# Kernel tuning notes

Hardware: AMD Instinct MI355X
Metric: run time of the kernel (lower is better)

Reference implementation:

```python
import jax, jax.numpy as jnp
import numpy as np
from jax import lax

D_INNER = 1024
D_STATE = 16
DT_RANK = 32


def conv2d(x, w, b, pad=1):
    y = lax.conv_general_dilated(x, w, (1, 1), [(pad, pad), (pad, pad)],
                                 dimension_numbers=('NCHW', 'OIHW', 'NCHW'))
    return y + b[None, :, None, None]


def maxpool2(x):
    return lax.reduce_window(x, -jnp.inf, lax.max, (1, 1, 2, 2), (1, 1, 2, 2), 'VALID')


def layer_norm(x, w, b, eps=1e-5):
    m = x.mean(-1, keepdims=True)
    v = ((x - m) ** 2).mean(-1, keepdims=True)
    return (x - m) * lax.rsqrt(v + eps) * w + b


def cblock(h, w1, b1, w2, b2):
    return jax.nn.relu(conv2d(jax.nn.relu(conv2d(h, w1, b1)), w2, b2))


def up2(d, w, b):
    # ConvTranspose2d(kernel=2, stride=2): each input pixel -> 2x2 output block
    Bn, Ci, H, W = d.shape
    y = jnp.einsum('bcij,copq->boipjq', d, w).reshape(Bn, w.shape[1], 2 * H, 2 * W)
    return y + b[None, :, None, None]


def eblock(e, d, upw, upb, w1, b1, w2, b2):
    d = up2(d, upw, upb)
    dy = e.shape[2] - d.shape[2]
    dx = e.shape[3] - d.shape[3]
    e = e[:, :, dy // 2:e.shape[2] - dy // 2, dx // 2:e.shape[3] - dx // 2]
    return cblock(jnp.concatenate([e, d], 1), w1, b1, w2, b2)


def mamba(hs, inW, cw, cb, xpW, dtW, dtB, Alog, Dp, outW):
    # standard Mamba-1 mixer: in_proj -> causal depthwise conv -> selective scan -> gate -> out_proj
    Bn, L, _ = hs.shape
    xz = jnp.einsum('bld,ed->ble', hs, inW)                       # [B,L,2*d_inner]
    xi, z = xz[..., :D_INNER], xz[..., D_INNER:]
    xc = lax.conv_general_dilated(xi.transpose(0, 2, 1), cw[:, None, :], (1,), [(3, 0)],
                                  dimension_numbers=('NCH', 'OIH', 'NCH'),
                                  feature_group_count=D_INNER)    # causal, len L
    xc = jax.nn.silu(xc + cb[None, :, None]).transpose(0, 2, 1)   # [B,L,d_inner]
    xdbl = jnp.einsum('bld,ed->ble', xc, xpW)                     # [B,L,dt_rank+2*d_state]
    dt = jax.nn.softplus(jnp.einsum('blr,dr->bld', xdbl[..., :DT_RANK], dtW) + dtB)
    Bs = xdbl[..., DT_RANK:DT_RANK + D_STATE]
    Cs = xdbl[..., DT_RANK + D_STATE:]
    A = -jnp.exp(Alog)                                            # [d_inner,d_state]
    dA = jnp.exp(dt[..., None] * A)                               # [B,L,d_inner,d_state]
    dBu = (dt * xc)[..., None] * Bs[:, :, None, :]

    def step(h, inp):
        dA_t, dBu_t, C_t = inp
        h = dA_t * h + dBu_t
        return h, jnp.einsum('bdn,bn->bd', h, C_t)

    h0 = jnp.zeros((Bn, D_INNER, D_STATE), hs.dtype)
    _, ys = lax.scan(step, h0, (dA.transpose(1, 0, 2, 3), dBu.transpose(1, 0, 2, 3), Cs.transpose(1, 0, 2)))
    y = ys.transpose(1, 0, 2) + Dp * xc
    return jnp.einsum('ble,de->bld', y * jax.nn.silu(z), outW)


def setup_inputs() -> dict:
    key = jax.random.key(0)
    ks = iter(jax.random.split(key, 80))

    def w(shape, fan_in):
        return jax.random.normal(next(ks), shape, jnp.float32) * np.float32(np.sqrt(2.0 / fan_in))

    H = W = 128
    fy = np.fft.fftfreq(H)
    fx = np.fft.fftfreq(W)
    r = np.sqrt(fy[:, None] ** 2 + fx[None, :] ** 2)
    r = r / r.max()
    bands = [(0.0, 0.15), (0.15, 0.35), (0.35, 1.0001)]
    freq_masks = jnp.asarray(np.stack([((r >= lo) & (r < hi)).astype(np.float32) for lo, hi in bands]))

    d = {}
    d['x'] = jax.random.normal(next(ks), (2, 1, H, W), jnp.float32)
    d['freq_masks'] = freq_masks
    for ci, co, n in [(3, 64, 'e1'), (64, 128, 'e2'), (128, 256, 'e3'), (256, 512, 'e4')]:
        d[n + 'w1'] = w((co, ci, 3, 3), ci * 9)
        d[n + 'b1'] = jnp.zeros((co,), jnp.float32)
        d[n + 'w2'] = w((co, co, 3, 3), co * 9)
        d[n + 'b2'] = jnp.zeros((co,), jnp.float32)
    d['cls_token'] = jnp.zeros((1, 1, 512), jnp.float32)
    d['norm_w'] = jnp.ones((24, 512), jnp.float32)
    d['norm_b'] = jnp.zeros((24, 512), jnp.float32)
    d['in_proj_w'] = w((24, 2048, 512), 512)
    d['conv1d_w'] = w((24, 1024, 4), 4)
    d['conv1d_b'] = jnp.zeros((24, 1024), jnp.float32)
    d['x_proj_w'] = w((24, 64, 1024), 1024)
    d['dt_w'] = w((24, 1024, 32), 32)
    d['dt_b'] = jnp.full((24, 1024), float(np.log(np.expm1(0.01))), jnp.float32)
    d['A_log'] = jnp.broadcast_to(jnp.log(jnp.arange(1, 17, dtype=jnp.float32)), (24, 1024, 16)) + 0.0
    d['D_ssm'] = jnp.ones((24, 1024), jnp.float32)
    d['out_proj_w'] = w((24, 512, 1024), 1024)
    for n, ci, co, cc in [('d4', 512, 256, 768), ('d3', 256, 128, 384), ('d2', 128, 64, 192), ('d1', 64, 32, 96)]:
        d[n + 'up_w'] = w((ci, co, 2, 2), ci * 4)
        d[n + 'up_b'] = jnp.zeros((co,), jnp.float32)
        d[n + 'w1'] = w((co, cc, 3, 3), cc * 9)
        d[n + 'b1'] = jnp.zeros((co,), jnp.float32)
        d[n + 'w2'] = w((co, co, 3, 3), co * 9)
        d[n + 'b2'] = jnp.zeros((co,), jnp.float32)
    d['final_w'] = w((4, 32, 1, 1), 32)
    d['final_b'] = jnp.zeros((4,), jnp.float32)
    return d


def reference(x, freq_masks, e1w1, e1b1, e1w2, e1b2, e2w1, e2b1, e2w2, e2b2,
              e3w1, e3b1, e3w2, e3b2, e4w1, e4b1, e4w2, e4b2, cls_token,
              norm_w, norm_b, in_proj_w, conv1d_w, conv1d_b, x_proj_w, dt_w, dt_b,
              A_log, D_ssm, out_proj_w,
              d4up_w, d4up_b, d4w1, d4b1, d4w2, d4b2,
              d3up_w, d3up_b, d3w1, d3b1, d3w2, d3b2,
              d2up_w, d2up_b, d2w1, d2b1, d2w2, d2b2,
              d1up_w, d1up_b, d1w1, d1b1, d1w2, d1b2,
              final_w, final_b):
    # DCT/FFT frequency split: [B,1,H,W] -> [B,3,H,W]
    xf = jnp.fft.fft2(x)
    x_freq = jnp.real(jnp.fft.ifft2(xf * freq_masks[None]))

    e1 = cblock(x_freq, e1w1, e1b1, e1w2, e1b2); p1 = maxpool2(e1)
    e2 = cblock(p1, e2w1, e2b1, e2w2, e2b2); p2 = maxpool2(e2)
    e3 = cblock(p2, e3w1, e3b1, e3w2, e3b2); p3 = maxpool2(e3)
    e4 = cblock(p3, e4w1, e4b1, e4w2, e4b2); p4 = maxpool2(e4)   # [B,512,H/16,W/16]

    Bn, _, Hs, Ws = p4.shape
    seq = p4.reshape(Bn, 512, Hs * Ws).transpose(0, 2, 1)
    tok = jnp.concatenate([jnp.broadcast_to(cls_token, (Bn, 1, 512)), seq], 1)

    params = (norm_w, norm_b, in_proj_w, conv1d_w, conv1d_b, x_proj_w, dt_w, dt_b, A_log, D_ssm, out_proj_w)

    def layer(carry, p):
        hidden, residual = carry
        nw, nb, inW, cw, cb, xpW, dtW, dtB, Alog, Dp, outW = p
        residual = residual + hidden   # first block: residual starts == hidden (faithful)
        hs = layer_norm(residual, nw, nb)
        hs = mamba(hs, inW, cw, cb, xpW, dtW, dtB, Alog, Dp, outW)
        return (hs, residual), None

    (hidden, _), _ = lax.scan(layer, (tok, tok), params)

    xsp = hidden[:, 1:, :].transpose(0, 2, 1).reshape(Bn, 512, Hs, Ws)

    d4 = eblock(e4, xsp, d4up_w, d4up_b, d4w1, d4b1, d4w2, d4b2)
    d3 = eblock(e3, d4, d3up_w, d3up_b, d3w1, d3b1, d3w2, d3b2)
    d2 = eblock(e2, d3, d2up_w, d2up_b, d2w1, d2b1, d2w2, d2b2)
    d1 = eblock(e1, d2, d1up_w, d1up_b, d1w1, d1b1, d1w2, d1b2)

    out = conv2d(d1, final_w, final_b, pad=0)
    out = jax.image.resize(out, (out.shape[0], out.shape[1], out.shape[2] * 16, out.shape[3] * 16), 'bilinear')
    return out
```

## Files before the change

kernel.cpp:

```cpp
#include <hip/hip_runtime.h>
#include <math.h>

#define PI_F 3.14159265358979323846f
typedef _Float16 f16;
typedef __attribute__((ext_vector_type(8))) _Float16 f16x8;
typedef __attribute__((ext_vector_type(4))) float f32x4;

__device__ __forceinline__ float siluf(float x){ return x / (1.f + expf(-x)); }
__device__ __forceinline__ float softplusf(float x){ return fmaxf(x,0.f) + log1pf(expf(-fabsf(x))); }
__device__ __forceinline__ void f2hl(float v, f16& hi, f16& lo){
  hi = (f16)v;
  lo = (f16)(v - (float)hi);
}

__global__ void k_dft_rows(const float* __restrict__ x, float* __restrict__ Tre, float* __restrict__ Tim){
  int v = threadIdx.x; int y = blockIdx.x; int b = blockIdx.y;
  __shared__ float cs[128], sn[128];
  float ang = -2.f*PI_F*(float)v/128.f;
  cs[v]=cosf(ang); sn[v]=sinf(ang);
  __syncthreads();
  const float* row = x + (b*128+y)*128;
  float re=0.f, im=0.f;
  for(int n=0;n<128;n++){ float xv=row[n]; int ph=(v*n)&127; re=fmaf(xv,cs[ph],re); im=fmaf(xv,sn[ph],im); }
  int o=(b*128+y)*128+v; Tre[o]=re; Tim[o]=im;
}
__global__ void k_dft_cols(const float* __restrict__ Tre, const float* __restrict__ Tim,
                           float* __restrict__ Fre, float* __restrict__ Fim){
  int v=threadIdx.x; int u=blockIdx.x; int b=blockIdx.y;
  __shared__ float cs[128], sn[128];
  float ang=-2.f*PI_F*(float)v/128.f; cs[v]=cosf(ang); sn[v]=sinf(ang);
  __syncthreads();
  float re=0.f,im=0.f;
  for(int y=0;y<128;y++){
    int ph=(u*y)&127; float c=cs[ph], s=sn[ph];
    int o=(b*128+y)*128+v;
    float tr=Tre[o], ti=Tim[o];
    re += tr*c - ti*s; im += tr*s + ti*c;
  }
  int o=(b*128+u)*128+v; Fre[o]=re; Fim[o]=im;
}
__global__ void k_idft_cols(const float* __restrict__ Fre,const float* __restrict__ Fim,
                            const float* __restrict__ mask, float* __restrict__ Gre,float* __restrict__ Gim){
  int v=threadIdx.x; int y=blockIdx.x; int m=blockIdx.y; int b=blockIdx.z;
  __shared__ float cs[128], sn[128];
  float ang=-2.f*PI_F*(float)v/128.f; cs[v]=cosf(ang); sn[v]=sinf(ang);
  __syncthreads();
  float re=0.f,im=0.f;
  for(int u=0;u<128;u++){
    int ph=(u*y)&127; float c=cs[ph], s=sn[ph];
    float w = mask[(m*128+u)*128+v];
    int o=(b*128+u)*128+v;
    float fr=Fre[o]*w, fi=Fim[o]*w;
    re += fr*c + fi*s;
    im += fi*c - fr*s;
  }
  int o=((b*3+m)*128+y)*128+v;
  Gre[o]=re*(1.f/128.f); Gim[o]=im*(1.f/128.f);
}
__global__ void k_idft_rows(const float* __restrict__ Gre,const float* __restrict__ Gim, float* __restrict__ xf){
  int xc=threadIdx.x; int y=blockIdx.x; int m=blockIdx.y; int b=blockIdx.z;
  __shared__ float cs[128], sn[128];
  float ang=-2.f*PI_F*(float)xc/128.f; cs[xc]=cosf(ang); sn[xc]=sinf(ang);
  __syncthreads();
  float re=0.f;
  const float* gr=Gre+((b*3+m)*128+y)*128;
  const float* gi=Gim+((b*3+m)*128+y)*128;
  for(int v=0;v<128;v++){
    int ph=(v*xc)&127;
    re += gr[v]*cs[ph] + gi[v]*sn[ph];
  }
  xf[((b*3+m)*128+y)*128+xc] = re*(1.f/128.f);
}

__global__ void k_w2hl(const float* __restrict__ w, f16* __restrict__ dh, f16* __restrict__ dl,
                       int N, int K, int Kp){
  int k = blockIdx.x*256 + threadIdx.x;
  int n = blockIdx.y;
  if (k >= Kp) return;
  float v = (n < N && k < K) ? w[(size_t)n*K + k] : 0.f;
  f16 h,l; f2hl(v,h,l);
  dh[(size_t)n*Kp + k] = h; dl[(size_t)n*Kp + k] = l;
}
__global__ void k_upw2hl(const float* __restrict__ w, f16* __restrict__ dh, f16* __restrict__ dl,
                         int Co, int K, int Kp){
  int k = blockIdx.x*256 + threadIdx.x;
  int n = blockIdx.y;
  if (k >= Kp) return;
  int o = n>>2, p=(n>>1)&1, q=n&1;
  float v = (k < K) ? w[(((size_t)k*Co + o)*2 + p)*2 + q] : 0.f;
  f16 h,l; f2hl(v,h,l);
  dh[(size_t)n*Kp + k] = h; dl[(size_t)n*Kp + k] = l;
}

__global__ void k_im2col(const float* __restrict__ in1, int C1, const float* __restrict__ in2, int C2,
                         int H, int W, int wsh, int hwsh, int K, int Kp, int m0, int ks3,
                         f16* __restrict__ Ah, f16* __restrict__ Al){
  int k = blockIdx.x*256 + threadIdx.x;
  int lm = blockIdx.y;
  if (k >= Kp) return;
  float val = 0.f;
  if (k < K){
    int ci, dy, dx;
    if (ks3){ ci = k/9; int tt = k - ci*9; int r3 = tt/3; dy = r3 - 1; dx = tt - r3*3 - 1; }
    else { ci = k; dy = 0; dx = 0; }
    int m = m0 + lm;
    int b = m >> hwsh;
    int hw = m & ((1<<hwsh)-1);
    int y = (hw >> wsh) + dy;
    int x = (hw & (W-1)) + dx;
    if (y >= 0 && y < H && x >= 0 && x < W){
      val = (ci < C1) ? in1[(((size_t)b*C1 + ci)*H + y)*W + x]
                      : in2[(((size_t)b*C2 + (ci-C1))*H + y)*W + x];
    }
  }
  f16 h,l; f2hl(val,h,l);
  Ah[(size_t)lm*Kp + k] = h; Al[(size_t)lm*Kp + k] = l;
}

__global__ void k_wcvt4(const float* __restrict__ wi, const float* __restrict__ wx,
                        const float* __restrict__ wdt, const float* __restrict__ wo,
                        f16* __restrict__ wih, f16* __restrict__ wil,
                        f16* __restrict__ wxh, f16* __restrict__ wxl,
                        f16* __restrict__ wdh, f16* __restrict__ wdl,
                        f16* __restrict__ woh, f16* __restrict__ wol){
  int i = blockIdx.x*256 + threadIdx.x;
  f16 h,l;
  if (i < 1048576){
    f2hl(wi[i],h,l); wih[i]=h; wil[i]=l;
  } else if (i < 1114112){
    int j = i - 1048576; f2hl(wx[j],h,l); wxh[j]=h; wxl[j]=l;
  } else if (i < 1179648){
    int j = i - 1114112; int n=j>>6, k=j&63;
    float v = (k<32) ? wdt[n*32+k] : 0.f;
    f2hl(v,h,l); wdh[j]=h; wdl[j]=l;
  } else if (i < 1703936){
    int j = i - 1179648; f2hl(wo[j],h,l); woh[j]=h; wol[j]=l;
  }
}

__global__ void k_zero_pads(f16* hsh, f16* hsl, f16* xch, f16* xcl,
                            f16* xdh, f16* xdl, f16* gth, f16* gtl){
  int i = blockIdx.x*256 + threadIdx.x;
  if (i >= 62*2624) return;
  int r = 130 + i/2624, c = i%2624;
  if (c < 512){ hsh[r*512+c]=(f16)0.f; hsl[r*512+c]=(f16)0.f; }
  else if (c < 1536){ int k=c-512; xch[r*1024+k]=(f16)0.f; xcl[r*1024+k]=(f16)0.f; }
  else if (c < 1600){ int k=c-1536; xdh[r*64+k]=(f16)0.f; xdl[r*64+k]=(f16)0.f; }
  else { int k=c-1600; gth[r*1024+k]=(f16)0.f; gtl[r*1024+k]=(f16)0.f; }
}

#define GLLDS(gp, ls) __builtin_amdgcn_global_load_lds( \
    (const __attribute__((address_space(1))) void*)(gp), \
    (__attribute__((address_space(3))) void*)(ls), 16, 0, 0)

__global__ __launch_bounds__(256) void k_gemm_hl(
    const f16* __restrict__ Wh, const f16* __restrict__ Wl,
    const f16* __restrict__ Ph, const f16* __restrict__ Pl,
    const float* __restrict__ bias, float* __restrict__ out,
    int N, int Kp, int m0, int wsh, int hwsh, int Co, int act, int mode,
    int Mreal, int ldc, f16* __restrict__ ehi, f16* __restrict__ elo)
{
  __shared__ __align__(16) f16 sm[3*4*2048];
  int bn = blockIdx.y*64;
  int bm = blockIdx.x*64;
  int t = threadIdx.x;
  int lane = t & 63, wv = t >> 6;
  int wr = wv >> 1, wc = wv & 1;

  float bv[2][4];
  {
    int cb = bn + wr*32 + (lane>>4)*4;
    #pragma unroll
    for (int ri=0;ri<2;ri++)
      #pragma unroll
      for (int r=0;r<4;r++){
        int co = cb + ri*16 + r;
        int idx = (mode==1) ? (co>>2) : co;
        int lim = (mode==1) ? (N>>2) : N;
        if (idx >= lim) idx = lim-1;
        bv[ri][r] = bias ? bias[idx] : 0.f;
      }
  }
  asm volatile("s_waitcnt vmcnt(0)" ::: "memory");

  int rr = lane >> 2;
  int cg = (lane & 3) ^ ((lane >> 3) & 3);
  size_t gW = (size_t)(bn + wv*16 + rr)*Kp + cg*8;
  size_t gP = (size_t)(bm + wv*16 + rr)*Kp + cg*8;
  int lb = wv*512;

  int rA = lane & 15, c = lane >> 4;
  int RW = wr*32 + rA; int sW = (RW>>1)&3;
  int offW = RW*32 + 8*(c ^ sW);
  int RP = wc*32 + rA; int sP = (RP>>1)&3;
  int offP = RP*32 + 8*(c ^ sP);

  f32x4 zz = {0.f,0.f,0.f,0.f};
  f32x4 acc[2][2];
  acc[0][0]=zz; acc[0][1]=zz; acc[1][0]=zz; acc[1][1]=zz;

  auto stage = [&](int bfi, int kk){
    GLLDS(Wh + gW + kk, &sm[(bfi*4+0)*2048 + lb]);
    GLLDS(Wl + gW + kk, &sm[(bfi*4+1)*2048 + lb]);
    GLLDS(Ph + gP + kk, &sm[(bfi*4+2)*2048 + lb]);
    GLLDS(Pl + gP + kk, &sm[(bfi*4+3)*2048 + lb]);
  };

  int nt = Kp >> 5;
  stage(0, 0);
  stage(1, (nt>1)?32:0);
  stage(2, (nt>2)?64:0);

  for (int tt = 0; tt < nt; ++tt){
    asm volatile("s_waitcnt vmcnt(8)" ::: "memory");
    __builtin_amdgcn_s_barrier();
    asm volatile("" ::: "memory");
    int bfi = tt % 3;
    int base = bfi*8192;
    f16x8 w0h = *(const f16x8*)&sm[base + offW];
    f16x8 w1h = *(const f16x8*)&sm[base + offW + 512];
    f16x8 w0l = *(const f16x8*)&sm[base + 2048 + offW];
    f16x8 w1l = *(const f16x8*)&sm[base + 2048 + offW + 512];
    f16x8 p0h = *(const f16x8*)&sm[base + 4096 + offP];
    f16x8 p1h = *(const f16x8*)&sm[base + 4096 + offP + 512];
    f16x8 p0l = *(const f16x8*)&sm[base + 6144 + offP];
    f16x8 p1l = *(const f16x8*)&sm[base + 6144 + offP + 512];
    acc[0][0] = __builtin_amdgcn_mfma_f32_16x16x32_f16(w0h, p0h, acc[0][0], 0,0,0);
    acc[0][1] = __builtin_amdgcn_mfma_f32_16x16x32_f16(w0h, p1h, acc[0][1], 0,0,0);
    acc[1][0] = __builtin_amdgcn_mfma_f32_16x16x32_f16(w1h, p0h, acc[1][0], 0,0,0);
    acc[1][1] = __builtin_amdgcn_mfma_f32_16x16x32_f16(w1h, p1h, acc[1][1], 0,0,0);
    acc[0][0] = __builtin_amdgcn_mfma_f32_16x16x32_f16(w0h, p0l, acc[0][0], 0,0,0);
    acc[0][1] = __builtin_amdgcn_mfma_f32_16x16x32_f16(w0h, p1l, acc[0][1], 0,0,0);
    acc[1][0] = __builtin_amdgcn_mfma_f32_16x16x32_f16(w1h, p0l, acc[1][0], 0,0,0);
    acc[1][1] = __builtin_amdgcn_mfma_f32_16x16x32_f16(w1h, p1l, acc[1][1], 0,0,0);
    acc[0][0] = __builtin_amdgcn_mfma_f32_16x16x32_f16(w0l, p0h, acc[0][0], 0,0,0);
    acc[0][1] = __builtin_amdgcn_mfma_f32_16x16x32_f16(w0l, p1h, acc[0][1], 0,0,0);
    acc[1][0] = __builtin_amdgcn_mfma_f32_16x16x32_f16(w1l, p0h, acc[1][0], 0,0,0);
    acc[1][1] = __builtin_amdgcn_mfma_f32_16x16x32_f16(w1l, p1h, acc[1][1], 0,0,0);
    __builtin_amdgcn_s_barrier();
    asm volatile("" ::: "memory");
    int kn = (tt+3 < nt) ? (tt+3)*32 : 0;
    stage(bfi, kn);
  }

  int HW = 1<<hwsh;
  int Wi = 1<<wsh;
  int Hi = 1<<(hwsh-wsh);
  #pragma unroll
  for (int ri=0;ri<2;ri++)
  #pragma unroll
  for (int ci=0;ci<2;ci++)
  #pragma unroll
  for (int r=0;r<4;r++){
    int co = bn + wr*32 + ri*16 + (lane>>4)*4 + r;
    int pm = bm + wc*32 + ci*16 + (lane&15);
    if (co < N){
      float v = acc[ri][ci][r];
      int m = m0 + pm;
      if (mode == 0){
        v += bv[ri][r];
        if (act == 2) v = fmaxf(v, 0.f);
        int b = m >> hwsh;
        int hw = m & (HW-1);
        out[((size_t)b*Co + co)*HW + hw] = v;
      } else if (mode == 1){
        int o = co>>2, p=(co>>1)&1, q=co&1;
        v += bv[ri][r];
        int b = m >> hwsh;
        int ij = m & (HW-1);
        int i = ij >> wsh, j = ij & (Wi-1);
        out[(((size_t)b*Co + o)*(2*Hi) + 2*i+p)*(2*Wi) + 2*j+q] = v;
      } else {
        if (m < Mreal){
          v += bv[ri][r];
          if (act == 1) v = softplusf(v);
          else if (act == 2) v = fmaxf(v, 0.f);
          out[(size_t)m*ldc + co] = v;
          if (ehi){
            f16 h,l; f2hl(v,h,l);
            ehi[(size_t)m*ldc + co] = h;
            elo[(size_t)m*ldc + co] = l;
          }
        }
      }
    }
  }
}

__global__ void k_maxpool2(const float* __restrict__ in, float* __restrict__ out, int BC, int H, int W){
  int Ho=H/2, Wo=W/2;
  int idx = blockIdx.x*blockDim.x + threadIdx.x;
  if (idx >= BC*Ho*Wo) return;
  int xo = idx % Wo; int yo = (idx / Wo) % Ho; int c = idx / (Wo*Ho);
  const float* p = in + ((size_t)c*H + 2*yo)*W + 2*xo;
  out[idx] = fmaxf(fmaxf(p[0],p[1]), fmaxf(p[W],p[W+1]));
}

__global__ void k_build_tok(const float* __restrict__ p4, const float* __restrict__ cls,
                            float* __restrict__ hidden, float* __restrict__ residual){
  int idx = blockIdx.x*blockDim.x+threadIdx.x;
  if (idx >= 2*65*512) return;
  int d = idx % 512; int l = (idx/512)%65; int b = idx/(512*65);
  float v = (l==0) ? cls[d] : p4[((size_t)b*512+d)*64 + (l-1)];
  hidden[idx]=v; residual[idx]=v;
}

__global__ void k_add_ln(float* __restrict__ residual, const float* __restrict__ hidden,
                         const float* __restrict__ nw, const float* __restrict__ nb,
                         f16* __restrict__ hsh, f16* __restrict__ hsl){
  int row = blockIdx.x;
  int t = threadIdx.x;
  __shared__ float red[256];
  size_t base = (size_t)row*512;
  float v0 = residual[base + t]       + hidden[base + t];
  float v1 = residual[base + 256 + t] + hidden[base + 256 + t];
  residual[base+t]=v0; residual[base+256+t]=v1;
  red[t]=v0+v1; __syncthreads();
  for(int o=128;o>0;o>>=1){ if(t<o) red[t]+=red[t+o]; __syncthreads(); }
  float mean = red[0]/512.f; __syncthreads();
  float d0=v0-mean, d1=v1-mean;
  red[t]=d0*d0+d1*d1; __syncthreads();
  for(int o=128;o>0;o>>=1){ if(t<o) red[t]+=red[t+o]; __syncthreads(); }
  float rstd = rsqrtf(red[0]/512.f + 1e-5f);
  float a = d0*rstd*nw[t]     + nb[t];
  float b = d1*rstd*nw[256+t] + nb[256+t];
  f16 h,l;
  f2hl(a,h,l); hsh[base+t]=h;     hsl[base+t]=l;
  f2hl(b,h,l); hsh[base+256+t]=h; hsl[base+256+t]=l;
}

__global__ void k_conv1d_silu(const float* __restrict__ xz, const float* __restrict__ cw,
                              const float* __restrict__ cb, float* __restrict__ xc,
                              f16* __restrict__ xch, f16* __restrict__ xcl){
  int d = blockIdx.x*blockDim.x + threadIdx.x;
  int l = blockIdx.y, b = blockIdx.z;
  if (d>=1024) return;
  float acc = cb[d];
  #pragma unroll
  for(int k=0;k<4;k++){
    int lp = l-3+k;
    if (lp>=0) acc = fmaf(xz[((size_t)(b*65+lp))*2048 + d], cw[d*4+k], acc);
  }
  float v = siluf(acc);
  size_t o = ((size_t)(b*65+l))*1024 + d;
  xc[o] = v;
  f16 h,ll; f2hl(v,h,ll); xch[o]=h; xcl[o]=ll;
}

__global__ void k_scan(const float* __restrict__ dt, const float* __restrict__ xc,
                       const float* __restrict__ xdbl, const float* __restrict__ xz,
                       const float* __restrict__ Alog, const float* __restrict__ Dp,
                       f16* __restrict__ gth, f16* __restrict__ gtl){
  int gid = blockIdx.x*blockDim.x + threadIdx.x;
  if (gid >= 2*1024*16) return;
  int n = gid & 15;
  int d = (gid >> 4) & 1023;
  int b = gid >> 14;
  float A = -expf(Alog[d*16+n]);
  float Dv = Dp[d];
  float h = 0.f;
  for (int l=0;l<65;l++){
    size_t r = (size_t)(b*65+l);
    float dtv = dt[r*1024+d];
    float xcv = xc[r*1024+d];
    float Bn = xdbl[r*64 + 32 + n];
    float Cn = xdbl[r*64 + 48 + n];
    h = fmaf(expf(dtv*A), h, dtv*xcv*Bn);
    float y = h*Cn;
    y += __shfl_xor(y, 1); y += __shfl_xor(y, 2);
    y += __shfl_xor(y, 4); y += __shfl_xor(y, 8);
    if (n==0){
      float zv = xz[r*2048 + 1024 + d];
      float g = (y + Dv*xcv) * siluf(zv);
      f16 hh,lo; f2hl(g,hh,lo);
      gth[r*1024+d]=hh; gtl[r*1024+d]=lo;
    }
  }
}

__global__ void k_xsp(const float* __restrict__ hidden, float* __restrict__ xsp){
  int idx = blockIdx.x*blockDim.x+threadIdx.x;
  if (idx>=2*512*64) return;
  int j = idx & 63; int c = (idx>>6)&511; int b = idx>>15;
  xsp[idx] = hidden[((size_t)(b*65 + 1 + j))*512 + c];
}

__global__ void k_conv1x1(const float* __restrict__ in, const float* __restrict__ w,
                          const float* __restrict__ bias, float* __restrict__ out){
  int hw = blockIdx.x*blockDim.x+threadIdx.x; if (hw>=128*128) return;
  int o = blockIdx.y, b = blockIdx.z;
  float acc = bias[o];
  #pragma unroll
  for(int c=0;c<32;c++) acc = fmaf(in[((size_t)(b*32+c))*16384 + hw], w[o*32+c], acc);
  out[((size_t)(b*4+o))*16384 + hw] = acc;
}

__global__ void k_resize16(const float* __restrict__ in, float* __restrict__ out){
  size_t idx = (size_t)blockIdx.x*blockDim.x + threadIdx.x;
  if (idx >= (size_t)2*4*2048*2048) return;
  int x = idx & 2047; int y = (int)((idx>>11)&2047); int c = (int)(idx>>22);
  float sx = ((float)x+0.5f)*(1.f/16.f) - 0.5f;
  float sy = ((float)y+0.5f)*(1.f/16.f) - 0.5f;
  int x0 = (int)floorf(sx); float fx = sx-(float)x0;
  int y0 = (int)floorf(sy); float fy = sy-(float)y0;
  int x0c = max(x0,0), x1c = min(x0+1,127);
  int y0c = max(y0,0), y1c = min(y0+1,127);
  const float* p = in + (size_t)c*16384;
  float v00=p[y0c*128+x0c], v01=p[y0c*128+x1c], v10=p[y1c*128+x0c], v11=p[y1c*128+x1c];
  out[idx] = (1.f-fy)*((1.f-fx)*v00 + fx*v01) + fy*((1.f-fx)*v10 + fx*v11);
}

#define MAX_A_ELEMS (16384*576)
#define MAX_B_ELEMS (512*4608)

extern "C" void kernel_launch(void* const* d_in, const int* in_sizes, int n_in,
                              void* d_out, int out_size, void* d_ws, size_t ws_size,
                              hipStream_t stream) {
  const float* x        = (const float*)d_in[0];
  const float* masks    = (const float*)d_in[1];
  const float* ew1[4] = {(const float*)d_in[2],(const float*)d_in[6],(const float*)d_in[10],(const float*)d_in[14]};
  const float* eb1[4] = {(const float*)d_in[3],(const float*)d_in[7],(const float*)d_in[11],(const float*)d_in[15]};
  const float* ew2[4] = {(const float*)d_in[4],(const float*)d_in[8],(const float*)d_in[12],(const float*)d_in[16]};
  const float* eb2[4] = {(const float*)d_in[5],(const float*)d_in[9],(const float*)d_in[13],(const float*)d_in[17]};
  const float* cls      = (const float*)d_in[18];
  const float* norm_w   = (const float*)d_in[19];
  const float* norm_b   = (const float*)d_in[20];
  const float* in_proj  = (const float*)d_in[21];
  const float* conv1d_w = (const float*)d_in[22];
  const float* conv1d_b = (const float*)d_in[23];
  const float* x_proj   = (const float*)d_in[24];
  const float* dt_w     = (const float*)d_in[25];
  const float* dt_b     = (const float*)d_in[26];
  const float* A_log    = (const float*)d_in[27];
  const float* D_ssm    = (const float*)d_in[28];
  const float* out_proj = (const float*)d_in[29];
  const float* dup_w[4] = {(const float*)d_in[30],(const float*)d_in[36],(const float*)d_in[42],(const float*)d_in[48]};
  const float* dup_b[4] = {(const float*)d_in[31],(const float*)d_in[37],(const float*)d_in[43],(const float*)d_in[49]};
  const float* dw1[4]   = {(const float*)d_in[32],(const float*)d_in[38],(const float*)d_in[44],(const float*)d_in[50]};
  const float* db1[4]   = {(const float*)d_in[33],(const float*)d_in[39],(const float*)d_in[45],(const float*)d_in[51]};
  const float* dw2[4]   = {(const float*)d_in[34],(const float*)d_in[40],(const float*)d_in[46],(const float*)d_in[52]};
  const float* db2[4]   = {(const float*)d_in[35],(const float*)d_in[41],(const float*)d_in[47],(const float*)d_in[53]};
  const float* final_w  = (const float*)d_in[54];
  const float* final_b  = (const float*)d_in[55];
  float* out = (float*)d_out;

  float* W = (float*)d_ws;
  size_t off = 0;
  auto alloc = [&](size_t n){ float* p = W + off; off += n; return p; };

  float* Tre = alloc(32768);  float* Tim = alloc(32768);
  float* Fre = alloc(32768);  float* Fim = alloc(32768);
  float* Gre = alloc(196608); float* Gim = alloc(196608);
  float* xfreq = alloc(98304);
  float* tmpA = alloc(2097152);
  float* e1 = alloc(2097152);
  float* p1 = alloc(524288);
  float* e2 = alloc(1048576);
  float* p2 = alloc(262144);
  float* e3 = alloc(524288);
  float* p3 = alloc(131072);
  float* e4 = alloc(262144);
  float* p4 = alloc(65536);
  float* hidden   = alloc(66560);
  float* residual = alloc(66560);
  float* xz  = alloc(266240);
  float* xc  = alloc(133120);
  float* xdbl= alloc(8320);
  float* dtb = alloc(133120);
  float* xsp = alloc(65536);
  float* tmpB = alloc(1048576);
  float* d4 = alloc(131072);
  float* d3 = alloc(262144);
  float* d2 = alloc(524288);
  float* d1 = alloc(1048576);
  float* fin = alloc(131072);
  (void)ws_size; (void)n_in; (void)in_sizes; (void)out_size;

  f16* q = (f16*)d_out;
  f16* Ahi = q; q += MAX_A_ELEMS;
  f16* Alo = q; q += MAX_A_ELEMS;
  f16* Bhi = q; q += MAX_B_ELEMS;
  f16* Blo = q; q += MAX_B_ELEMS;
  f16* wi_h = q; q += 1048576;  f16* wi_l = q; q += 1048576;
  f16* wx_h = q; q += 65536;    f16* wx_l = q; q += 65536;
  f16* wdt_h = q; q += 65536;   f16* wdt_l = q; q += 65536;
  f16* wo_h = q; q += 524288;   f16* wo_l = q; q += 524288;
  f16* hs_h = q; q += 98304;    f16* hs_l = q; q += 98304;
  f16* xc_h = q; q += 196608;   f16* xc_l = q; q += 196608;
  f16* xd_h = q; q += 12288;    f16* xd_l = q; q += 12288;
  f16* gt_h = q; q += 196608;   f16* gt_l = q; q += 196608;

  hipLaunchKernelGGL(k_dft_rows, dim3(128,2), dim3(128), 0, stream, x, Tre, Tim);
  hipLaunchKernelGGL(k_dft_cols, dim3(128,2), dim3(128), 0, stream, Tre, Tim, Fre, Fim);
  hipLaunchKernelGGL(k_idft_cols, dim3(128,3,2), dim3(128), 0, stream, Fre, Fim, masks, Gre, Gim);
  hipLaunchKernelGGL(k_idft_rows, dim3(128,3,2), dim3(128), 0, stream, Gre, Gim, xfreq);

  auto ctz = [](int v){ int s=0; while(!(v&1)){v>>=1;s++;} return s; };
  auto conv_bf = [&](const float* i1,int C1,const float* i2,int C2,
                     const float* w,const float* bias, float* o,
                     int Co,int H,int Wd){
    int Ci=C1+C2, K=Ci*9, Kp=(K+31)&~31, Np=(Co+63)&~63;
    int M=2*H*Wd;
    int wsh=ctz(Wd), hwsh=ctz(H*Wd);
    hipLaunchKernelGGL(k_w2hl, dim3((Kp+255)/256, Np), dim3(256), 0, stream, w, Bhi, Blo, Co, K, Kp);
    int maxRows = (MAX_A_ELEMS / Kp) & ~63;
    for (int m0=0; m0<M; m0+=maxRows){
      int mc = M-m0 < maxRows ? M-m0 : maxRows;
      hipLaunchKernelGGL(k_im2col, dim3((Kp+255)/256, mc), dim3(256), 0, stream,
                         i1, C1, i2, C2, H, Wd, wsh, hwsh, K, Kp, m0, 1, Ahi, Alo);
      hipLaunchKernelGGL(k_gemm_hl, dim3(mc/64, Np/64), dim3(256), 0, stream,
                         Bhi, Blo, Ahi, Alo, bias, o, Co, Kp, m0, wsh, hwsh, Co, 2, 0,
                         1<<30, 0, (f16*)nullptr, (f16*)nullptr);
    }
  };
  auto up_bf = [&](const float* in,const float* w,const float* bias,float* o,
                   int Ci,int Co,int Hi){
    int Kp=Ci, N=4*Co;
    int M=2*Hi*Hi;
    int wsh=ctz(Hi), hwsh=ctz(Hi*Hi);
    hipLaunchKernelGGL(k_upw2hl, dim3((Kp+255)/256, N), dim3(256), 0, stream, w, Bhi, Blo, Co, Ci, Kp);
    hipLaunchKernelGGL(k_im2col, dim3((Kp+255)/256, M), dim3(256), 0, stream,
                       in, Ci, (const float*)nullptr, 0, Hi, Hi, wsh, hwsh, Ci, Kp, 0, 0, Ahi, Alo);
    hipLaunchKernelGGL(k_gemm_hl, dim3(M/64, N/64), dim3(256), 0, stream,
                       Bhi, Blo, Ahi, Alo, bias, o, N, Kp, 0, wsh, hwsh, Co, 0, 1,
                       1<<30, 0, (f16*)nullptr, (f16*)nullptr);
  };

  conv_bf(xfreq,3,  nullptr,0, ew1[0], eb1[0], tmpA, 64, 128,128);
  conv_bf(tmpA,64,  nullptr,0, ew2[0], eb2[0], e1,   64, 128,128);
  hipLaunchKernelGGL(k_maxpool2, dim3((2*64*64*64+255)/256), dim3(256), 0, stream, e1, p1, 2*64, 128,128);
  conv_bf(p1,64,    nullptr,0, ew1[1], eb1[1], tmpA, 128, 64,64);
  conv_bf(tmpA,128, nullptr,0, ew2[1], eb2[1], e2,   128, 64,64);
  hipLaunchKernelGGL(k_maxpool2, dim3((2*128*32*32+255)/256), dim3(256), 0, stream, e2, p2, 2*128, 64,64);
  conv_bf(p2,128,   nullptr,0, ew1[2], eb1[2], tmpA, 256, 32,32);
  conv_bf(tmpA,256, nullptr,0, ew2[2], eb2[2], e3,   256, 32,32);
  hipLaunchKernelGGL(k_maxpool2, dim3((2*256*16*16+255)/256), dim3(256), 0, stream, e3, p3, 2*256, 32,32);
  conv_bf(p3,256,   nullptr,0, ew1[3], eb1[3], tmpA, 512, 16,16);
  conv_bf(tmpA,512, nullptr,0, ew2[3], eb2[3], e4,   512, 16,16);
  hipLaunchKernelGGL(k_maxpool2, dim3((2*512*8*8+255)/256), dim3(256), 0, stream, e4, p4, 2*512, 16,16);

  hipLaunchKernelGGL(k_build_tok, dim3((2*65*512+255)/256), dim3(256), 0, stream, p4, cls, hidden, residual);
  hipLaunchKernelGGL(k_zero_pads, dim3((62*2624+255)/256), dim3(256), 0, stream,
                     hs_h, hs_l, xc_h, xc_l, xd_h, xd_l, gt_h, gt_l);
  auto mgemm = [&](const f16* wh, const f16* wl, const f16* ph, const f16* pl,
                   const float* bias, float* o, int N, int Kp, int act,
                   f16* eh, f16* el){
    hipLaunchKernelGGL(k_gemm_hl, dim3(3, N/64), dim3(256), 0, stream,
                       wh, wl, ph, pl, bias, o, N, Kp, 0, 0, 0, 0, act, 2,
                       130, N, eh, el);
  };
  for (int l=0;l<24;l++){
    const float* nw   = norm_w   + (size_t)l*512;
    const float* nb   = norm_b   + (size_t)l*512;
    const float* inW  = in_proj  + (size_t)l*2048*512;
    const float* cw   = conv1d_w + (size_t)l*1024*4;
    const float* cb   = conv1d_b + (size_t)l*1024;
    const float* xpW  = x_proj   + (size_t)l*64*1024;
    const float* dtW  = dt_w     + (size_t)l*1024*32;
    const float* dtB  = dt_b     + (size_t)l*1024;
    const float* Alg  = A_log    + (size_t)l*1024*16;
    const float* Dp   = D_ssm    + (size_t)l*1024;
    const float* outW = out_proj + (size_t)l*512*1024;

    hipLaunchKernelGGL(k_wcvt4, dim3((1703936+255)/256), dim3(256), 0, stream,
                       inW, xpW, dtW, outW, wi_h, wi_l, wx_h, wx_l, wdt_h, wdt_l, wo_h, wo_l);
    hipLaunchKernelGGL(k_add_ln, dim3(130), dim3(256), 0, stream, residual, hidden, nw, nb, hs_h, hs_l);
    mgemm(wi_h, wi_l, hs_h, hs_l, nullptr, xz, 2048, 512, 0, nullptr, nullptr);
    hipLaunchKernelGGL(k_conv1d_silu, dim3(4,65,2), dim3(256), 0, stream, xz, cw, cb, xc, xc_h, xc_l);
    mgemm(wx_h, wx_l, xc_h, xc_l, nullptr, xdbl, 64, 1024, 0, xd_h, xd_l);
    mgemm(wdt_h, wdt_l, xd_h, xd_l, dtB, dtb, 1024, 64, 1, nullptr, nullptr);
    hipLaunchKernelGGL(k_scan, dim3(128), dim3(256), 0, stream, dtb, xc, xdbl, xz, Alg, Dp, gt_h, gt_l);
    mgemm(wo_h, wo_l, gt_h, gt_l, nullptr, hidden, 512, 1024, 0, nullptr, nullptr);
  }
  hipLaunchKernelGGL(k_xsp, dim3((2*512*64+255)/256), dim3(256), 0, stream, hidden, xsp);

  up_bf(xsp, dup_w[0], dup_b[0], tmpB, 512, 256, 8);
  conv_bf(e4,512, tmpB,256, dw1[0], db1[0], tmpA, 256, 16,16);
  conv_bf(tmpA,256, nullptr,0, dw2[0], db2[0], d4, 256, 16,16);
  up_bf(d4, dup_w[1], dup_b[1], tmpB, 256, 128, 16);
  conv_bf(e3,256, tmpB,128, dw1[1], db1[1], tmpA, 128, 32,32);
  conv_bf(tmpA,128, nullptr,0, dw2[1], db2[1], d3, 128, 32,32);
  up_bf(d3, dup_w[2], dup_b[2], tmpB, 128, 64, 32);
  conv_bf(e2,128, tmpB,64, dw1[2], db1[2], tmpA, 64, 64,64);
  conv_bf(tmpA,64, nullptr,0, dw2[2], db2[2], d2, 64, 64,64);
  up_bf(d2, dup_w[3], dup_b[3], tmpB, 64, 32, 64);
  conv_bf(e1,64, tmpB,32, dw1[3], db1[3], tmpA, 32, 128,128);
  conv_bf(tmpA,32, nullptr,0, dw2[3], db2[3], d1, 32, 128,128);

  hipLaunchKernelGGL(k_conv1x1, dim3((16384+255)/256, 4, 2), dim3(256), 0, stream, d1, final_w, final_b, fin);
  hipLaunchKernelGGL(k_resize16, dim3((size_t)(2*4*2048*2048)/256), dim3(256), 0, stream, fin, out);
}
```

Before: 3.871 ms.

## Batch conv weight conversion and split fp32 Mamba weights inside GEMM

```diff
diff --git a/kernel.cpp b/kernel.cpp
--- a/kernel.cpp
+++ b/kernel.cpp
@@ -72,24 +72,33 @@
   xf[((b*3+m)*128+y)*128+xc] = re*(1.f/128.f);
 }
 
-__global__ void k_w2hl(const float* __restrict__ w, f16* __restrict__ dh, f16* __restrict__ dl,
-                       int N, int K, int Kp){
-  int k = blockIdx.x*256 + threadIdx.x;
-  int n = blockIdx.y;
-  if (k >= Kp) return;
-  float v = (n < N && k < K) ? w[(size_t)n*K + k] : 0.f;
+#define NWD 20
+struct WAll {
+  const float* src[NWD];
+  int N[NWD], K[NWD], Kp[NWD], up[NWD];
+  int cum[NWD+1];
+};
+__global__ void k_wcvt_all(WAll d, int total, f16* __restrict__ bh, f16* __restrict__ bl){
+  int gid = blockIdx.x*256 + threadIdx.x;
+  if (gid >= total) return;
+  int li = gid, N = d.N[0], K = d.K[0], Kp = d.Kp[0], up = d.up[0];
+  const float* src = d.src[0];
+  #pragma unroll
+  for (int j=1;j<NWD;j++){
+    if (gid >= d.cum[j]){
+      li = gid - d.cum[j]; N=d.N[j]; K=d.K[j]; Kp=d.Kp[j]; up=d.up[j]; src=d.src[j];
+    }
+  }
+  int n = li / Kp, k = li - n*Kp;
+  float v = 0.f;
+  if (up){
+    int o = n>>2, p=(n>>1)&1, q=n&1;
+    if (k < K) v = src[(((size_t)k*up + o)*2 + p)*2 + q];
+  } else {
+    if (n < N && k < K) v = src[(size_t)n*K + k];
+  }
   f16 h,l; f2hl(v,h,l);
-  dh[(size_t)n*Kp + k] = h; dl[(size_t)n*Kp + k] = l;
-}
-__global__ void k_upw2hl(const float* __restrict__ w, f16* __restrict__ dh, f16* __restrict__ dl,
-                         int Co, int K, int Kp){
-  int k = blockIdx.x*256 + threadIdx.x;
-  int n = blockIdx.y;
-  if (k >= Kp) return;
-  int o = n>>2, p=(n>>1)&1, q=n&1;
-  float v = (k < K) ? w[(((size_t)k*Co + o)*2 + p)*2 + q] : 0.f;
-  f16 h,l; f2hl(v,h,l);
-  dh[(size_t)n*Kp + k] = h; dl[(size_t)n*Kp + k] = l;
+  bh[gid]=h; bl[gid]=l;
 }
 
 __global__ void k_im2col(const float* __restrict__ in1, int C1, const float* __restrict__ in2, int C2,
@@ -117,27 +126,6 @@
   Ah[(size_t)lm*Kp + k] = h; Al[(size_t)lm*Kp + k] = l;
 }
 
-__global__ void k_wcvt4(const float* __restrict__ wi, const float* __restrict__ wx,
-                        const float* __restrict__ wdt, const float* __restrict__ wo,
-                        f16* __restrict__ wih, f16* __restrict__ wil,
-                        f16* __restrict__ wxh, f16* __restrict__ wxl,
-                        f16* __restrict__ wdh, f16* __restrict__ wdl,
-                        f16* __restrict__ woh, f16* __restrict__ wol){
-  int i = blockIdx.x*256 + threadIdx.x;
-  f16 h,l;
-  if (i < 1048576){
-    f2hl(wi[i],h,l); wih[i]=h; wil[i]=l;
-  } else if (i < 1114112){
-    int j = i - 1048576; f2hl(wx[j],h,l); wxh[j]=h; wxl[j]=l;
-  } else if (i < 1179648){
-    int j = i - 1114112; int n=j>>6, k=j&63;
-    float v = (k<32) ? wdt[n*32+k] : 0.f;
-    f2hl(v,h,l); wdh[j]=h; wdl[j]=l;
-  } else if (i < 1703936){
-    int j = i - 1179648; f2hl(wo[j],h,l); woh[j]=h; wol[j]=l;
-  }
-}
-
 __global__ void k_zero_pads(f16* hsh, f16* hsl, f16* xch, f16* xcl,
                             f16* xdh, f16* xdl, f16* gth, f16* gtl){
   int i = blockIdx.x*256 + threadIdx.x;
@@ -157,8 +145,7 @@
     const f16* __restrict__ Wh, const f16* __restrict__ Wl,
     const f16* __restrict__ Ph, const f16* __restrict__ Pl,
     const float* __restrict__ bias, float* __restrict__ out,
-    int N, int Kp, int m0, int wsh, int hwsh, int Co, int act, int mode,
-    int Mreal, int ldc, f16* __restrict__ ehi, f16* __restrict__ elo)
+    int N, int Kp, int m0, int wsh, int hwsh, int Co, int act, int mode)
 {
   __shared__ __align__(16) f16 sm[3*4*2048];
   int bn = blockIdx.y*64;
@@ -263,25 +250,131 @@
         int b = m >> hwsh;
         int hw = m & (HW-1);
         out[((size_t)b*Co + co)*HW + hw] = v;
-      } else if (mode == 1){
+      } else {
         int o = co>>2, p=(co>>1)&1, q=co&1;
         v += bv[ri][r];
         int b = m >> hwsh;
         int ij = m & (HW-1);
         int i = ij >> wsh, j = ij & (Wi-1);
         out[(((size_t)b*Co + o)*(2*Hi) + 2*i+p)*(2*Wi) + 2*j+q] = v;
-      } else {
-        if (m < Mreal){
-          v += bv[ri][r];
-          if (act == 1) v = softplusf(v);
-          else if (act == 2) v = fmaxf(v, 0.f);
-          out[(size_t)m*ldc + co] = v;
-          if (ehi){
-            f16 h,l; f2hl(v,h,l);
-            ehi[(size_t)m*ldc + co] = h;
-            elo[(size_t)m*ldc + co] = l;
-          }
-        }
+      }
+    }
+  }
+}
+
+__global__ __launch_bounds__(256) void k_gemm_w32(
+    const float* __restrict__ Wf, int ldaW,
+    const f16* __restrict__ Ph, const f16* __restrict__ Pl, int ldaP,
+    const float* __restrict__ bias, float* __restrict__ out,
+    int N, int Kp, int act, int Mreal, int ldc,
+    f16* __restrict__ ehi, f16* __restrict__ elo)
+{
+  __shared__ __align__(16) float smW[3*2048];
+  __shared__ __align__(16) f16 smP[3*2*2048];
+  int bn = blockIdx.y*64;
+  int bm = blockIdx.x*64;
+  int t = threadIdx.x;
+  int lane = t & 63, wv = t >> 6;
+  int wr = wv >> 1, wc = wv & 1;
+
+  float bv[2][4];
+  {
+    int cb = bn + wr*32 + (lane>>4)*4;
+    #pragma unroll
+    for (int ri=0;ri<2;ri++)
+      #pragma unroll
+      for (int r=0;r<4;r++)
+        bv[ri][r] = bias ? bias[cb + ri*16 + r] : 0.f;
+  }
+  asm volatile("s_waitcnt vmcnt(0)" ::: "memory");
+
+  int wcs = (lane & 7) ^ (lane >> 3);
+  size_t gWoff = (size_t)(bn + wv*16 + (lane>>3))*ldaW + wcs*4;
+  int prr = lane >> 2;
+  int pcg = (lane & 3) ^ ((lane >> 3) & 3);
+  size_t gPoff = (size_t)(bm + wv*16 + prr)*ldaP + pcg*8;
+
+  int rA = lane & 15, c = lane >> 4;
+  int RW0 = wr*32 + rA;  int swz = RW0 & 7;
+  int RP = wc*32 + rA;   int sP = (RP>>1)&3;
+  int offP = RP*32 + 8*(c ^ sP);
+  int cw0 = ((2*c)   ^ swz)*4;
+  int cw1 = ((2*c+1) ^ swz)*4;
+
+  f32x4 zz = {0.f,0.f,0.f,0.f};
+  f32x4 acc[2][2];
+  acc[0][0]=zz; acc[0][1]=zz; acc[1][0]=zz; acc[1][1]=zz;
+
+  auto stage = [&](int bfi, int kk){
+    GLLDS(Wf + gWoff + kk,              &smW[bfi*2048 + wv*512]);
+    GLLDS(Wf + gWoff + kk + 8*(size_t)ldaW, &smW[bfi*2048 + wv*512 + 256]);
+    GLLDS(Ph + gPoff + kk, &smP[bfi*4096 + wv*512]);
+    GLLDS(Pl + gPoff + kk, &smP[bfi*4096 + 2048 + wv*512]);
+  };
+
+  int nt = Kp >> 5;
+  stage(0, 0);
+  stage(1, (nt>1)?32:0);
+  stage(2, (nt>2)?64:0);
+
+  for (int tt = 0; tt < nt; ++tt){
+    asm volatile("s_waitcnt vmcnt(8)" ::: "memory");
+    __builtin_amdgcn_s_barrier();
+    asm volatile("" ::: "memory");
+    int bfi = tt % 3;
+    const float* bW = &smW[bfi*2048];
+    f32x4 a0 = *(const f32x4*)&bW[RW0*32 + cw0];
+    f32x4 a1 = *(const f32x4*)&bW[RW0*32 + cw1];
+    f32x4 a2 = *(const f32x4*)&bW[RW0*32 + 512 + cw0];
+    f32x4 a3 = *(const f32x4*)&bW[RW0*32 + 512 + cw1];
+    f16x8 w0h, w0l, w1h, w1l;
+    #pragma unroll
+    for (int j=0;j<4;j++){
+      f16 h;
+      h=(f16)a0[j]; w0h[j]=h;   w0l[j]  =(f16)(a0[j]-(float)h);
+      h=(f16)a1[j]; w0h[4+j]=h; w0l[4+j]=(f16)(a1[j]-(float)h);
+      h=(f16)a2[j]; w1h[j]=h;   w1l[j]  =(f16)(a2[j]-(float)h);
+      h=(f16)a3[j]; w1h[4+j]=h; w1l[4+j]=(f16)(a3[j]-(float)h);
+    }
+    const f16* bP = &smP[bfi*4096];
+    f16x8 p0h = *(const f16x8*)&bP[offP];
+    f16x8 p1h = *(const f16x8*)&bP[offP + 512];
+    f16x8 p0l = *(const f16x8*)&bP[2048 + offP];
+    f16x8 p1l = *(const f16x8*)&bP[2048 + offP + 512];
+    acc[0][0] = __builtin_amdgcn_mfma_f32_16x16x32_f16(w0h, p0h, acc[0][0], 0,0,0);
+    acc[0][1] = __builtin_amdgcn_mfma_f32_16x16x32_f16(w0h, p1h, acc[0][1], 0,0,0);
+    acc[1][0] = __builtin_amdgcn_mfma_f32_16x16x32_f16(w1h, p0h, acc[1][0], 0,0,0);
+    acc[1][1] = __builtin_amdgcn_mfma_f32_16x16x32_f16(w1h, p1h, acc[1][1], 0,0,0);
+    acc[0][0] = __builtin_amdgcn_mfma_f32_16x16x32_f16(w0h, p0l, acc[0][0], 0,0,0);
+    acc[0][1] = __builtin_amdgcn_mfma_f32_16x16x32_f16(w0h, p1l, acc[0][1], 0,0,0);
+    acc[1][0] = __builtin_amdgcn_mfma_f32_16x16x32_f16(w1h, p0l, acc[1][0], 0,0,0);
+    acc[1][1] = __builtin_amdgcn_mfma_f32_16x16x32_f16(w1h, p1l, acc[1][1], 0,0,0);
+    acc[0][0] = __builtin_amdgcn_mfma_f32_16x16x32_f16(w0l, p0h, acc[0][0], 0,0,0);
+    acc[0][1] = __builtin_amdgcn_mfma_f32_16x16x32_f16(w0l, p1h, acc[0][1], 0,0,0);
+    acc[1][0] = __builtin_amdgcn_mfma_f32_16x16x32_f16(w1l, p0h, acc[1][0], 0,0,0);
+    acc[1][1] = __builtin_amdgcn_mfma_f32_16x16x32_f16(w1l, p1h, acc[1][1], 0,0,0);
+    __builtin_amdgcn_s_barrier();
+    asm volatile("" ::: "memory");
+    int kn = (tt+3 < nt) ? (tt+3)*32 : 0;
+    stage(bfi, kn);
+  }
+
+  #pragma unroll
+  for (int ri=0;ri<2;ri++)
+  #pragma unroll
+  for (int ci=0;ci<2;ci++)
+  #pragma unroll
+  for (int r=0;r<4;r++){
+    int co = bn + wr*32 + ri*16 + (lane>>4)*4 + r;
+    int m  = bm + wc*32 + ci*16 + (lane&15);
+    if (m < Mreal){
+      float v = acc[ri][ci][r] + bv[ri][r];
+      if (act == 1) v = softplusf(v);
+      out[(size_t)m*ldc + co] = v;
+      if (ehi){
+        f16 h,l; f2hl(v,h,l);
+        ehi[(size_t)m*ldc + co] = h;
+        elo[(size_t)m*ldc + co] = l;
       }
     }
   }
@@ -411,7 +504,6 @@
 }
 
 #define MAX_A_ELEMS (16384*576)
-#define MAX_B_ELEMS (512*4608)
 
 extern "C" void kernel_launch(void* const* d_in, const int* in_sizes, int n_in,
                               void* d_out, int out_size, void* d_ws, size_t ws_size,
@@ -476,20 +568,38 @@
   float* fin = alloc(131072);
   (void)ws_size; (void)n_in; (void)in_sizes; (void)out_size;
 
+  WAll wa;
+  {
+    const float* s[NWD] = { ew1[0], ew2[0], ew1[1], ew2[1], ew1[2], ew2[2], ew1[3], ew2[3],
+                            dw1[0], dw2[0], dw1[1], dw2[1], dw1[2], dw2[2], dw1[3], dw2[3],
+                            dup_w[0], dup_w[1], dup_w[2], dup_w[3] };
+    const int N_[NWD] = {64,64,128,128,256,256,512,512, 256,256,128,128,64,64,32,32, 1024,512,256,128};
+    const int K_[NWD] = {27,576,576,1152,1152,2304,2304,4608, 6912,2304,3456,1152,1728,576,864,288, 512,256,128,64};
+    const int U_[NWD] = {0,0,0,0,0,0,0,0, 0,0,0,0,0,0,0,0, 256,128,64,32};
+    int cacc = 0;
+    for (int i=0;i<NWD;i++){
+      wa.src[i]=s[i]; wa.N[i]=N_[i]; wa.K[i]=K_[i];
+      wa.Kp[i]=(K_[i]+31)&~31; wa.up[i]=U_[i];
+      wa.cum[i]=cacc;
+      int Np=(N_[i]+63)&~63;
+      cacc += Np*wa.Kp[i];
+    }
+    wa.cum[NWD]=cacc;
+  }
+  int wtotal = wa.cum[NWD];
+
   f16* q = (f16*)d_out;
   f16* Ahi = q; q += MAX_A_ELEMS;
   f16* Alo = q; q += MAX_A_ELEMS;
-  f16* Bhi = q; q += MAX_B_ELEMS;
-  f16* Blo = q; q += MAX_B_ELEMS;
-  f16* wi_h = q; q += 1048576;  f16* wi_l = q; q += 1048576;
-  f16* wx_h = q; q += 65536;    f16* wx_l = q; q += 65536;
-  f16* wdt_h = q; q += 65536;   f16* wdt_l = q; q += 65536;
-  f16* wo_h = q; q += 524288;   f16* wo_l = q; q += 524288;
+  f16* Ball_h = q; q += wtotal;
+  f16* Ball_l = q; q += wtotal;
   f16* hs_h = q; q += 98304;    f16* hs_l = q; q += 98304;
   f16* xc_h = q; q += 196608;   f16* xc_l = q; q += 196608;
   f16* xd_h = q; q += 12288;    f16* xd_l = q; q += 12288;
   f16* gt_h = q; q += 196608;   f16* gt_l = q; q += 196608;
 
+  hipLaunchKernelGGL(k_wcvt_all, dim3((wtotal+255)/256), dim3(256), 0, stream, wa, wtotal, Ball_h, Ball_l);
+
   hipLaunchKernelGGL(k_dft_rows, dim3(128,2), dim3(128), 0, stream, x, Tre, Tim);
   hipLaunchKernelGGL(k_dft_cols, dim3(128,2), dim3(128), 0, stream, Tre, Tim, Fre, Fim);
   hipLaunchKernelGGL(k_idft_cols, dim3(128,3,2), dim3(128), 0, stream, Fre, Fim, masks, Gre, Gim);
@@ -497,57 +607,56 @@
 
   auto ctz = [](int v){ int s=0; while(!(v&1)){v>>=1;s++;} return s; };
   auto conv_bf = [&](const float* i1,int C1,const float* i2,int C2,
-                     const float* w,const float* bias, float* o,
+                     int widx, const float* bias, float* o,
                      int Co,int H,int Wd){
     int Ci=C1+C2, K=Ci*9, Kp=(K+31)&~31, Np=(Co+63)&~63;
     int M=2*H*Wd;
     int wsh=ctz(Wd), hwsh=ctz(H*Wd);
-    hipLaunchKernelGGL(k_w2hl, dim3((Kp+255)/256, Np), dim3(256), 0, stream, w, Bhi, Blo, Co, K, Kp);
+    const f16* bh = Ball_h + wa.cum[widx];
+    const f16* bl = Ball_l + wa.cum[widx];
     int maxRows = (MAX_A_ELEMS / Kp) & ~63;
     for (int m0=0; m0<M; m0+=maxRows){
       int mc = M-m0 < maxRows ? M-m0 : maxRows;
       hipLaunchKernelGGL(k_im2col, dim3((Kp+255)/256, mc), dim3(256), 0, stream,
                          i1, C1, i2, C2, H, Wd, wsh, hwsh, K, Kp, m0, 1, Ahi, Alo);
       hipLaunchKernelGGL(k_gemm_hl, dim3(mc/64, Np/64), dim3(256), 0, stream,
-                         Bhi, Blo, Ahi, Alo, bias, o, Co, Kp, m0, wsh, hwsh, Co, 2, 0,
-                         1<<30, 0, (f16*)nullptr, (f16*)nullptr);
+                         bh, bl, Ahi, Alo, bias, o, Co, Kp, m0, wsh, hwsh, Co, 2, 0);
     }
   };
-  auto up_bf = [&](const float* in,const float* w,const float* bias,float* o,
+  auto up_bf = [&](const float* in, int widx, const float* bias, float* o,
                    int Ci,int Co,int Hi){
     int Kp=Ci, N=4*Co;
     int M=2*Hi*Hi;
     int wsh=ctz(Hi), hwsh=ctz(Hi*Hi);
-    hipLaunchKernelGGL(k_upw2hl, dim3((Kp+255)/256, N), dim3(256), 0, stream, w, Bhi, Blo, Co, Ci, Kp);
+    const f16* bh = Ball_h + wa.cum[widx];
+    const f16* bl = Ball_l + wa.cum[widx];
     hipLaunchKernelGGL(k_im2col, dim3((Kp+255)/256, M), dim3(256), 0, stream,
                        in, Ci, (const float*)nullptr, 0, Hi, Hi, wsh, hwsh, Ci, Kp, 0, 0, Ahi, Alo);
     hipLaunchKernelGGL(k_gemm_hl, dim3(M/64, N/64), dim3(256), 0, stream,
-                       Bhi, Blo, Ahi, Alo, bias, o, N, Kp, 0, wsh, hwsh, Co, 0, 1,
-                       1<<30, 0, (f16*)nullptr, (f16*)nullptr);
+                       bh, bl, Ahi, Alo, bias, o, N, Kp, 0, wsh, hwsh, Co, 0, 1);
   };
 
-  conv_bf(xfreq,3,  nullptr,0, ew1[0], eb1[0], tmpA, 64, 128,128);
-  conv_bf(tmpA,64,  nullptr,0, ew2[0], eb2[0], e1,   64, 128,128);
+  conv_bf(xfreq,3,  nullptr,0, 0, eb1[0], tmpA, 64, 128,128);
+  conv_bf(tmpA,64,  nullptr,0, 1, eb2[0], e1,   64, 128,128);
   hipLaunchKernelGGL(k_maxpool2, dim3((2*64*64*64+255)/256), dim3(256), 0, stream, e1, p1, 2*64, 128,128);
-  conv_bf(p1,64,    nullptr,0, ew1[1], eb1[1], tmpA, 128, 64,64);
-  conv_bf(tmpA,128, nullptr,0, ew2[1], eb2[1], e2,   128, 64,64);
+  conv_bf(p1,64,    nullptr,0, 2, eb1[1], tmpA, 128, 64,64);
+  conv_bf(tmpA,128, nullptr,0, 3, eb2[1], e2,   128, 64,64);
   hipLaunchKernelGGL(k_maxpool2, dim3((2*128*32*32+255)/256), dim3(256), 0, stream, e2, p2, 2*128, 64,64);
-  conv_bf(p2,128,   nullptr,0, ew1[2], eb1[2], tmpA, 256, 32,32);
-  conv_bf(tmpA,256, nullptr,0, ew2[2], eb2[2], e3,   256, 32,32);
+  conv_bf(p2,128,   nullptr,0, 4, eb1[2], tmpA, 256, 32,32);
+  conv_bf(tmpA,256, nullptr,0, 5, eb2[2], e3,   256, 32,32);
   hipLaunchKernelGGL(k_maxpool2, dim3((2*256*16*16+255)/256), dim3(256), 0, stream, e3, p3, 2*256, 32,32);
-  conv_bf(p3,256,   nullptr,0, ew1[3], eb1[3], tmpA, 512, 16,16);
-  conv_bf(tmpA,512, nullptr,0, ew2[3], eb2[3], e4,   512, 16,16);
+  conv_bf(p3,256,   nullptr,0, 6, eb1[3], tmpA, 512, 16,16);
+  conv_bf(tmpA,512, nullptr,0, 7, eb2[3], e4,   512, 16,16);
   hipLaunchKernelGGL(k_maxpool2, dim3((2*512*8*8+255)/256), dim3(256), 0, stream, e4, p4, 2*512, 16,16);
 
   hipLaunchKernelGGL(k_build_tok, dim3((2*65*512+255)/256), dim3(256), 0, stream, p4, cls, hidden, residual);
   hipLaunchKernelGGL(k_zero_pads, dim3((62*2624+255)/256), dim3(256), 0, stream,
                      hs_h, hs_l, xc_h, xc_l, xd_h, xd_l, gt_h, gt_l);
-  auto mgemm = [&](const f16* wh, const f16* wl, const f16* ph, const f16* pl,
-                   const float* bias, float* o, int N, int Kp, int act,
+  auto mgemm = [&](const float* Wf, int ldaW, const f16* ph, const f16* pl, int ldaP,
+                   const float* bias, float* o, int N, int Kp, int act, int ldc,
                    f16* eh, f16* el){
-    hipLaunchKernelGGL(k_gemm_hl, dim3(3, N/64), dim3(256), 0, stream,
-                       wh, wl, ph, pl, bias, o, N, Kp, 0, 0, 0, 0, act, 2,
-                       130, N, eh, el);
+    hipLaunchKernelGGL(k_gemm_w32, dim3(3, N/64), dim3(256), 0, stream,
+                       Wf, ldaW, ph, pl, ldaP, bias, o, N, Kp, act, 130, ldc, eh, el);
   };
   for (int l=0;l<24;l++){
     const float* nw   = norm_w   + (size_t)l*512;
@@ -562,30 +671,28 @@
     const float* Dp   = D_ssm    + (size_t)l*1024;
     const float* outW = out_proj + (size_t)l*512*1024;
 
-    hipLaunchKernelGGL(k_wcvt4, dim3((1703936+255)/256), dim3(256), 0, stream,
-                       inW, xpW, dtW, outW, wi_h, wi_l, wx_h, wx_l, wdt_h, wdt_l, wo_h, wo_l);
     hipLaunchKernelGGL(k_add_ln, dim3(130), dim3(256), 0, stream, residual, hidden, nw, nb, hs_h, hs_l);
-    mgemm(wi_h, wi_l, hs_h, hs_l, nullptr, xz, 2048, 512, 0, nullptr, nullptr);
+    mgemm(inW, 512, hs_h, hs_l, 512, nullptr, xz, 2048, 512, 0, 2048, nullptr, nullptr);
     hipLaunchKernelGGL(k_conv1d_silu, dim3(4,65,2), dim3(256), 0, stream, xz, cw, cb, xc, xc_h, xc_l);
-    mgemm(wx_h, wx_l, xc_h, xc_l, nullptr, xdbl, 64, 1024, 0, xd_h, xd_l);
-    mgemm(wdt_h, wdt_l, xd_h, xd_l, dtB, dtb, 1024, 64, 1, nullptr, nullptr);
+    mgemm(xpW, 1024, xc_h, xc_l, 1024, nullptr, xdbl, 64, 1024, 0, 64, xd_h, xd_l);
+    mgemm(dtW, 32, xd_h, xd_l, 64, dtB, dtb, 1024, 32, 1, 1024, nullptr, nullptr);
     hipLaunchKernelGGL(k_scan, dim3(128), dim3(256), 0, stream, dtb, xc, xdbl, xz, Alg, Dp, gt_h, gt_l);
-    mgemm(wo_h, wo_l, gt_h, gt_l, nullptr, hidden, 512, 1024, 0, nullptr, nullptr);
+    mgemm(outW, 1024, gt_h, gt_l, 1024, nullptr, hidden, 512, 1024, 0, 512, nullptr, nullptr);
   }
   hipLaunchKernelGGL(k_xsp, dim3((2*512*64+255)/256), dim3(256), 0, stream, hidden, xsp);
 
-  up_bf(xsp, dup_w[0], dup_b[0], tmpB, 512, 256, 8);
-  conv_bf(e4,512, tmpB,256, dw1[0], db1[0], tmpA, 256, 16,16);
-  conv_bf(tmpA,256, nullptr,0, dw2[0], db2[0], d4, 256, 16,16);
-  up_bf(d4, dup_w[1], dup_b[1], tmpB, 256, 128, 16);
-  conv_bf(e3,256, tmpB,128, dw1[1], db1[1], tmpA, 128, 32,32);
-  conv_bf(tmpA,128, nullptr,0, dw2[1], db2[1], d3, 128, 32,32);
-  up_bf(d3, dup_w[2], dup_b[2], tmpB, 128, 64, 32);
-  conv_bf(e2,128, tmpB,64, dw1[2], db1[2], tmpA, 64, 64,64);
-  conv_bf(tmpA,64, nullptr,0, dw2[2], db2[2], d2, 64, 64,64);
-  up_bf(d2, dup_w[3], dup_b[3], tmpB, 64, 32, 64);
-  conv_bf(e1,64, tmpB,32, dw1[3], db1[3], tmpA, 32, 128,128);
-  conv_bf(tmpA,32, nullptr,0, dw2[3], db2[3], d1, 32, 128,128);
+  up_bf(xsp, 16, dup_b[0], tmpB, 512, 256, 8);
+  conv_bf(e4,512, tmpB,256, 8, db1[0], tmpA, 256, 16,16);
+  conv_bf(tmpA,256, nullptr,0, 9, db2[0], d4, 256, 16,16);
+  up_bf(d4, 17, dup_b[1], tmpB, 256, 128, 16);
+  conv_bf(e3,256, tmpB,128, 10, db1[1], tmpA, 128, 32,32);
+  conv_bf(tmpA,128, nullptr,0, 11, db2[1], d3, 128, 32,32);
+  up_bf(d3, 18, dup_b[2], tmpB, 128, 64, 32);
+  conv_bf(e2,128, tmpB,64, 12, db1[2], tmpA, 64, 64,64);
+  conv_bf(tmpA,64, nullptr,0, 13, db2[2], d2, 64, 64,64);
+  up_bf(d2, 19, dup_b[3], tmpB, 64, 32, 64);
+  conv_bf(e1,64, tmpB,32, 14, db1[3], tmpA, 32, 128,128);
+  conv_bf(tmpA,32, nullptr,0, 15, db2[3], d1, 32, 128,128);
 
   hipLaunchKernelGGL(k_conv1x1, dim3((16384+255)/256, 4, 2), dim3(256), 0, stream, d1, final_w, final_b, fin);
   hipLaunchKernelGGL(k_resize16, dim3((size_t)(2*4*2048*2048)/256), dim3(256), 0, stream, fin, out);
```

Result: slower. 4.510 ms (+16.5%).
